# Performance work log

Hardware: AMD Instinct MI355X
Metric: run time of the kernel (lower is better)

## Reference

```python
import jax, jax.numpy as jnp
import numpy as np

D, H, W = 40, 32, 88
BEV_H, BEV_W = 125, 125
X_MIN, X_MAX, DX = -50.0, 50.0, 0.8
Y_MIN, Y_MAX, DY = -50.0, 50.0, 0.8
Z_MIN, DZ = -10.0, 20.0


def _voxel_indices():
    """Replicates frustum creation + get_geometry + index computation.
    Returns (flat_idx, valid) each of shape (D, H, W). Faithful to the
    original's sequential in-place max() semantics."""
    # depth_grid = arange(1, 41, 1) + 1  -> 2..41
    depth = jnp.arange(1.0, 41.0, 1.0) + 1.0            # (D,)
    xs = jnp.linspace(0.0, W - 1.0, W)                  # (W,)
    ys = jnp.linspace(0.0, H - 1.0, H)                  # (H,)
    d = depth[:, None, None]                            # (D,1,1)
    xd = jnp.broadcast_to(xs[None, None, :] * d, (D, H, W))  # x*depth
    yd = jnp.broadcast_to(ys[None, :, None] * d, (D, H, W))  # y*depth
    zd = jnp.broadcast_to(d, (D, H, W))                       # depth
    # first points_d.max(): over columns (xd, yd, zd)
    max1 = jnp.maximum(xd.max(), jnp.maximum(yd.max(), zd.max()))
    gx = xd / max1 * (X_MAX - X_MIN) + X_MIN
    # second points_d.max(): column 0 was overwritten in-place by gx
    max2 = jnp.maximum(gx.max(), jnp.maximum(yd.max(), zd.max()))
    gy = yd / max2 * (Y_MAX - Y_MIN) + Y_MIN
    gz = zd
    # voxelize (torch .long() truncates; all values here are >= 0)
    ix = ((gx - X_MIN) / DX).astype(jnp.int32)
    iy = ((gy - Y_MIN) / DY).astype(jnp.int32)
    iz = ((gz - Z_MIN) / DZ).astype(jnp.int32)
    valid = (ix >= 0) & (ix < BEV_W) & (iy >= 0) & (iy < BEV_H) & (iz >= 0)
    flat_idx = jnp.where(valid, iy * BEV_W + ix, 0)
    return flat_idx, valid


def setup_inputs() -> dict:
    key = jax.random.key(0)
    k1, k2, k3, k4, k5 = jax.random.split(key, 5)
    B, N, C = 1, 6, 128
    return {
        "img_feat": jax.random.normal(k1, (B, N, C, H, W), dtype=jnp.float32),
        "depth_logits": jax.random.normal(k2, (B, N, D, H, W), dtype=jnp.float32),
        "rots": jax.random.normal(k3, (B, N, 3, 3), dtype=jnp.float32),
        "trans": jax.random.normal(k4, (B, N, 3), dtype=jnp.float32),
        "intrins": jax.random.normal(k5, (B, N, 3, 3), dtype=jnp.float32),
    }


def reference(img_feat, depth_logits, rots, trans, intrins):
    B, N, C, h, w = img_feat.shape
    depth_probs = jax.nn.softmax(depth_logits, axis=2)         # (B,N,D,H,W)
    # depth-weighted outer product: (B,N,D,H,W,C)
    feats = jnp.einsum('bnchw,bndhw->bndhwc', img_feat, depth_probs)
    flat_feats = feats.reshape(-1, C)                          # (B*N*D*H*W, C)
    flat_idx, valid = _voxel_indices()                         # (D,H,W)
    idx = jnp.broadcast_to(flat_idx[None, None], (B, N, D, h, w)).reshape(-1)
    msk = jnp.broadcast_to(valid[None, None], (B, N, D, h, w)).reshape(-1)
    flat_feats = jnp.where(msk[:, None], flat_feats, 0.0)
    bev = jax.ops.segment_sum(flat_feats, idx, num_segments=BEV_H * BEV_W)
    bev = bev.reshape(BEV_H, BEV_W, C)
    return jnp.transpose(bev, (2, 0, 1))[None]                 # (1, C, 125, 125)
```

## Files before the change

### kernel.cpp

```cpp
#include <hip/hip_runtime.h>


constexpr int D = 40, H = 32, W = 88, HW = H * W;
constexpr int C = 128, NCAM = 6;
constexpr int BEV = 125, NBINS = BEV * BEV;
constexpr int NCOLS = NCAM * HW;

typedef __attribute__((ext_vector_type(8))) unsigned short us8;
typedef __attribute__((ext_vector_type(4))) float f4;
typedef __attribute__((ext_vector_type(2))) float f2;

__device__ __forceinline__ unsigned short f2bf(float x) {
    unsigned u = __float_as_uint(x);
    return (unsigned short)((u + 0x7FFF + ((u >> 16) & 1)) >> 16);
}
__device__ __forceinline__ float b2f(unsigned short u) {
    return __uint_as_float(((unsigned)u) << 16);
}

struct Tabs { short XP[D][126]; short YP[D][126]; };
constexpr Tabs make_tabs() {
    Tabs t{};
    for (int d = 0; d < D; ++d) {
        int dep = d + 2;
        int cntx[126] = {};
        for (int w = 0; w < W; ++w) {
            float gx = (float)(w * dep) / 3567.0f * 100.0f - 50.0f;
            int ix = (int)((gx + 50.0f) / 0.8f);
            if (ix < 125) cntx[ix]++;
        }
        t.XP[d][0] = 0;
        for (int X = 0; X < 125; ++X) t.XP[d][X + 1] = (short)(t.XP[d][X] + cntx[X]);
        int cnty[126] = {};
        for (int h = 0; h < H; ++h) {
            float gy = (float)(h * dep) / 1271.0f * 100.0f - 50.0f;
            int iy = (int)((gy + 50.0f) / 0.8f);
            if (iy < 125) cnty[iy]++;
        }
        t.YP[d][0] = 0;
        for (int Y = 0; Y < 125; ++Y) t.YP[d][Y + 1] = (short)(t.YP[d][Y] + cnty[Y]);
    }
    return t;
}
constexpr Tabs g_tabs = make_tabs();
__device__ const Tabs g_tab = g_tabs;

struct SegTable { unsigned a[4096]; unsigned b[4096]; int n; };

constexpr SegTable make_segs() {
    SegTable S{};
    int ns = 0;
    for (int iy = 0; iy < 125; ++iy) {
        int cnt[125] = {};
        for (int d = 0; d < D; ++d) {
            int yc = g_tabs.YP[d][iy + 1] - g_tabs.YP[d][iy];
            if (yc == 0) continue;
            for (int X = 0; X < 125; ++X)
                cnt[X] += (g_tabs.XP[d][X + 1] - g_tabs.XP[d][X]) * yc;
        }
        int X = 0;
        while (X < 125) {
            if (cnt[X] > 176) {
                int d0 = 0;
                while (d0 < D) {
                    int run = 0, d1 = d0;
                    while (d1 < D) {
                        int piece = (g_tabs.XP[d1][X + 1] - g_tabs.XP[d1][X]) *
                                    (g_tabs.YP[d1][iy + 1] - g_tabs.YP[d1][iy]);
                        if (d1 > d0 && run + piece > 128) break;
                        run += piece; ++d1;
                    }
                    if (run > 0) {
                        S.a[ns] = ((unsigned)iy << 16) | ((unsigned)X << 8) | (unsigned)(X + 1);
                        S.b[ns] = (1u << 31) | ((unsigned)d0 << 25) | ((unsigned)d1 << 19) | (unsigned)run;
                        ++ns;
                    }
                    d0 = d1;
                }
                ++X;
            } else {
                int X0 = X, run = 0;
                while (X < 125 && (X - X0) < 16 && cnt[X] <= 176 &&
                       (X == X0 || run + cnt[X] <= 128)) {
                    run += cnt[X]; ++X;
                }
                if (run > 0) {
                    S.a[ns] = ((unsigned)iy << 16) | ((unsigned)X0 << 8) | (unsigned)X;
                    S.b[ns] = ((unsigned)0 << 25) | ((unsigned)D << 19) | (unsigned)run;
                    ++ns;
                }
            }
        }
    }
    S.n = ns;
    return S;
}
constexpr SegTable g_raw = make_segs();

constexpr SegTable reorder_segs() {
    SegTable R{};
    int pos = 0;
    for (int i = 0; i < g_raw.n; ++i)
        if ((int)(g_raw.b[i] & 0x7FFFF) >= 120) { R.a[pos] = g_raw.a[i]; R.b[pos] = g_raw.b[i]; ++pos; }
    for (int i = 0; i < g_raw.n; ++i)
        if ((int)(g_raw.b[i] & 0x7FFFF) <  120) { R.a[pos] = g_raw.a[i]; R.b[pos] = g_raw.b[i]; ++pos; }
    R.n = pos;
    return R;
}
constexpr SegTable g_ct = reorder_segs();
constexpr int NSEG = g_ct.n;
static_assert(NSEG > 0 && NSEG <= 4096, "seg table overflow");
__device__ const SegTable g_segs = g_ct;

struct Meta { unsigned m[4096]; int ne; };
constexpr Meta make_meta() {
    Meta M{};
    int pos = 0;
    for (int i = 0; i < NSEG; ++i) {
        int cnt = (int)(g_ct.b[i] & 0x7FFFF);
        int ng = (((cnt + 1) >> 1) + 3) >> 2;
        M.m[i] = (g_ct.b[i] & 0x80000000u) | ((unsigned)pos << 10) | (unsigned)ng;
        pos += 2 * ng * 4;
    }
    M.ne = pos;
    return M;
}
constexpr Meta g_mt = make_meta();
constexpr int NE_TOT = g_mt.ne;
static_assert(NE_TOT < (1 << 21), "start field overflow");
struct MetaArr { unsigned m[4096]; };
constexpr MetaArr make_meta_arr() { MetaArr A{}; for (int i = 0; i < 4096; ++i) A.m[i] = g_mt.m[i]; return A; }
__device__ const MetaArr g_metaD = make_meta_arr();

__device__ __align__(16) unsigned g_glist[NE_TOT + 64];

constexpr int SMAX_BLOCKS  = NCOLS / 256;
constexpr int BUILD_BLOCKS = (NSEG + 3) / 4;
constexpr int PACK_BLOCKS  = (C / 8) * (HW / 32);
constexpr int ZERO_TOTAL   = C * NBINS / 4;
constexpr int ZERO_BLOCKS  = (ZERO_TOTAL + 1023) / 1024;
constexpr int MEGA_BLOCKS  = SMAX_BLOCKS + BUILD_BLOCKS + PACK_BLOCKS + ZERO_BLOCKS;

__global__ void __launch_bounds__(256) mega_kernel(
        const float* __restrict__ feat,
        const float* __restrict__ logits,
        float* __restrict__ probs_t,
        unsigned short* __restrict__ feat_p,
        float* __restrict__ out) {
    __shared__ __align__(16) float tile[NCAM * 8 * 37];
    int b = blockIdx.x, t = threadIdx.x;

    if (b < SMAX_BLOCKS) {
        int col = b * 256 + t;
        int n  = col / HW;
        int hw = col - n * HW;
        const float* src = logits + ((size_t)n * D) * HW + hw;
        float m = -3.402823466e+38f;
#pragma unroll 20
        for (int d = 0; d < D; ++d)
            m = fmaxf(m, src[(size_t)d * HW]);
        float s = 0.f;
#pragma unroll 8
        for (int d = 0; d < D; ++d)
            s += expf(src[(size_t)d * HW] - m);
        float inv = 1.0f / s;
#pragma unroll 8
        for (int d = 0; d < D; ++d)
            probs_t[(size_t)((d << 12) | hw) * 8 + n] =
                expf(src[(size_t)d * HW] - m) * inv;

    } else if (b < SMAX_BLOCKS + BUILD_BLOCKS) {
        int slot = (b - SMAX_BLOCKS) * 4 + (t >> 6);
        int lane = t & 63;
        if (slot < NSEG) {
            unsigned da = g_segs.a[slot], db = g_segs.b[slot], mb = g_metaD.m[slot];
            int iy = (int)(da >> 16), X0 = (int)((da >> 8) & 0xFF), X1 = (int)(da & 0xFF);
            int d0 = (int)((db >> 25) & 0x3F), d1 = (int)((db >> 19) & 0x3F);
            int drange = d1 - d0;
            int ng4 = (int)(mb & 0x3FFu) * 4;
            unsigned* gl = g_glist + ((mb >> 10) & 0x1FFFFFu);
            int base = 0;
            for (int bl = 0; bl < X1 - X0; ++bl) {
                int d = d0 + lane;
                int hb = 0, he = 0, wb = 0, we = 0, cnt = 0;
                if (lane < drange) {
                    hb = g_tab.YP[d][iy];      he = g_tab.YP[d][iy + 1];
                    wb = g_tab.XP[d][X0 + bl]; we = g_tab.XP[d][X0 + bl + 1];
                    cnt = (he - hb) * (we - wb);
                }
                int inc = cnt;
#pragma unroll
                for (int delta = 1; delta < 64; delta <<= 1) {
                    int y = __shfl_up(inc, delta, 64);
                    if (lane >= delta) inc += y;
                }
                int tot = __shfl(inc, 63, 64);
                int o = base + inc - cnt;
                int run_end = base + tot;
                for (int h = hb; h < he; ++h)
                    for (int w = wb; w < we; ++w) {
                        unsigned v = ((unsigned)bl << 19) | ((unsigned)d << 12)
                                   | (unsigned)(h * W + w);
                        if (o >= run_end - 2) v |= 0x80000000u;
                        gl[(o & 1) * ng4 + (o >> 1)] = v;
                        ++o;
                    }
                base = run_end;
            }
            int m = base;
#pragma unroll
            for (int dg = 0; dg < 2; ++dg) {
                int cnt2 = (m + 1 - dg) >> 1;
                for (int k = cnt2 + lane; k < ng4; k += 64)
                    gl[dg * ng4 + k] = (16u << 19) | 0x80000000u;
            }
        }

    } else if (b < SMAX_BLOCKS + BUILD_BLOCKS + PACK_BLOCKS) {
        int bb = b - SMAX_BLOCKS - BUILD_BLOCKS;
        int c0  = (bb / 88) * 8;
        int hw0 = (bb % 88) * 32;
        int cq = t >> 5, hwL = t & 31;
#pragma unroll
        for (int n = 0; n < NCAM; ++n)
            tile[(n * 8 + cq) * 37 + hwL] =
                feat[((size_t)(n * C + c0 + cq)) * HW + hw0 + hwL];
        __syncthreads();
        int hl = t >> 3, cL = t & 7;
        us8 v;
#pragma unroll
        for (int n = 0; n < NCAM; ++n)
            v[n] = f2bf(tile[(n * 8 + cL) * 37 + hl]);
        v[6] = 0; v[7] = 0;
        *(us8*)(feat_p + ((size_t)(hw0 + hl) * C + (c0 + cL)) * 8) = v;

    } else {
        int base = (b - SMAX_BLOCKS - BUILD_BLOCKS - PACK_BLOCKS) * 1024;
#pragma unroll
        for (int k = 0; k < 4; ++k) {
            int i = base + k * 256 + t;
            if (i < ZERO_TOTAL) ((f4*)out)[i] = f4{0.f, 0.f, 0.f, 0.f};
        }
    }
}

__global__ void __launch_bounds__(128, 4) gather_kernel(
        const unsigned short* __restrict__ feat_p,
        const float* __restrict__ probs_t,
        float* __restrict__ out) {
    __shared__ __align__(16) float T[2][17][66];
    __shared__ __align__(16) unsigned EL[192];
    int t = threadIdx.x;
    int slot = blockIdx.x >> 1, chalf = blockIdx.x & 1;
    unsigned da = g_segs.a[slot], mb = g_metaD.m[slot];
    int iy = (int)(da >> 16), X0 = (int)((da >> 8) & 0xFF), X1 = (int)(da & 0xFF);
    int width = X1 - X0;
    bool split = (mb >> 31) != 0;
    int ng = (int)(mb & 0x3FFu);
    unsigned start = (mb >> 10) & 0x1FFFFFu;
    int dg = __builtin_amdgcn_readfirstlane((int)(threadIdx.x >> 6));
    int lane = t & 63;
    int c = chalf * 64 + lane;
    int ntot = ng * 8;

    if (t < ntot) EL[t] = g_glist[start + (unsigned)t];
    if (t + 128 < ntot) EL[t + 128] = g_glist[start + (unsigned)(t + 128)];
    { float* Tf = &T[0][0][0];
      for (int i = t; i < 2 * 17 * 66; i += 128) Tf[i] = 0.f; }
    __syncthreads();

    const unsigned* ep = EL + dg * ng * 4;
    const unsigned short* fbase = feat_p + (size_t)c * 8;
    float* Tp = &T[dg][0][0];
    float racc = 0.f;

#define LOADE(E, g_) { uint4 ee_ = *(const uint4*)(ep + 4 * (g_));            \
    E[0] = (unsigned)__builtin_amdgcn_readfirstlane((int)ee_.x);              \
    E[1] = (unsigned)__builtin_amdgcn_readfirstlane((int)ee_.y);              \
    E[2] = (unsigned)__builtin_amdgcn_readfirstlane((int)ee_.z);              \
    E[3] = (unsigned)__builtin_amdgcn_readfirstlane((int)ee_.w); }
#define ISSUE(S, E) _Pragma("unroll") for (int i_ = 0; i_ < 4; ++i_) {        \
    fv##S[i_] = *(const us8*)(fbase + ((size_t)(E[i_] & 0xFFFu) << 10));      \
    const float* pp_ = probs_t + ((size_t)(E[i_] & 0x3FFFFu) << 3);           \
    pa##S[i_] = *(const f4*)pp_; pb##S[i_] = *(const f2*)(pp_ + 4); }
#define CONS(S, E) _Pragma("unroll") for (int i_ = 0; i_ < 4; ++i_) {         \
    racc += pa##S[i_].x * b2f(fv##S[i_][0]) + pa##S[i_].y * b2f(fv##S[i_][1]) \
          + pa##S[i_].z * b2f(fv##S[i_][2]) + pa##S[i_].w * b2f(fv##S[i_][3]) \
          + pb##S[i_].x * b2f(fv##S[i_][4]) + pb##S[i_].y * b2f(fv##S[i_][5]);\
    if (E[i_] & 0x80000000u) {                                                \
        Tp[((E[i_] >> 19) & 31u) * 66 + (unsigned)lane] += racc; racc = 0.f; } }

    unsigned EA[4], EB[4], ET[4];
    us8 fvA[4], fvB[4];
    f4 paA[4], paB[4];
    f2 pbA[4], pbB[4];
    LOADE(EA, 0); LOADE(EB, 1);
    ISSUE(A, EA);
    int g = 0;
    for (; g + 2 <= ng; g += 2) {
        ISSUE(B, EB);
        LOADE(ET, g + 2);
        CONS(A, EA);
        if (g + 2 < ng) {
            ISSUE(A, ET);
#pragma unroll
            for (int q = 0; q < 4; ++q) EA[q] = ET[q];
        }
        CONS(B, EB);
        LOADE(EB, g + 3);
    }
    if (g < ng) CONS(A, EA);
#undef LOADE
#undef ISSUE
#undef CONS
    __syncthreads();

    int binbase = iy * BEV + X0;
#pragma unroll
    for (int it = 0; it < 8; ++it) {
        int bl = t & 15, cc = it * 8 + (t >> 4);
        if (bl < width) {
            float v = T[0][bl][cc] + T[1][bl][cc];
            float* dst = &out[(size_t)(chalf * 64 + cc) * NBINS + binbase + bl];
            if (split) atomicAdd(dst, v);
            else       *dst = v;
        }
    }
}

extern "C" void kernel_launch(void* const* d_in, const int* in_sizes, int n_in,
                              void* d_out, int out_size, void* d_ws, size_t ws_size,
                              hipStream_t stream) {
    const float* img_feat     = (const float*)d_in[0];
    const float* depth_logits = (const float*)d_in[1];
    float* out = (float*)d_out;

    char* p = (char*)d_ws;
    float*          probs_t = (float*)p;          p += (size_t)D * 4096 * 8 * 4;
    unsigned short* feat_p  = (unsigned short*)p; p += (size_t)HW * C * 8 * 2;

    mega_kernel<<<MEGA_BLOCKS, 256, 0, stream>>>(
        img_feat, depth_logits, probs_t, feat_p, out);
    gather_kernel<<<NSEG * 2, 128, 0, stream>>>(feat_p, probs_t, out);
}
```

Measured before the change: 107.8 us.

## Pack bf16 features to 12 bytes and triple-buffer gather loads

```diff
diff --git a/kernel.cpp b/kernel.cpp
--- a/kernel.cpp
+++ b/kernel.cpp
@@ -13,9 +13,6 @@
 __device__ __forceinline__ unsigned short f2bf(float x) {
     unsigned u = __float_as_uint(x);
     return (unsigned short)((u + 0x7FFF + ((u >> 16) & 1)) >> 16);
-}
-__device__ __forceinline__ float b2f(unsigned short u) {
-    return __uint_as_float(((unsigned)u) << 16);
 }
 
 struct Tabs { short XP[D][126]; short YP[D][126]; };
@@ -227,12 +224,15 @@
                 feat[((size_t)(n * C + c0 + cq)) * HW + hw0 + hwL];
         __syncthreads();
         int hl = t >> 3, cL = t & 7;
-        us8 v;
+        unsigned short v[6];
 #pragma unroll
         for (int n = 0; n < NCAM; ++n)
             v[n] = f2bf(tile[(n * 8 + cL) * 37 + hl]);
-        v[6] = 0; v[7] = 0;
-        *(us8*)(feat_p + ((size_t)(hw0 + hl) * C + (c0 + cL)) * 8) = v;
+        unsigned* dst = (unsigned*)(feat_p +
+            ((size_t)(hw0 + hl) * C + (c0 + cL)) * 6);
+        dst[0] = (unsigned)v[0] | ((unsigned)v[1] << 16);
+        dst[1] = (unsigned)v[2] | ((unsigned)v[3] << 16);
+        dst[2] = (unsigned)v[4] | ((unsigned)v[5] << 16);
 
     } else {
         int base = (b - SMAX_BLOCKS - BUILD_BLOCKS - PACK_BLOCKS) * 1024;
@@ -244,7 +244,7 @@
     }
 }
 
-__global__ void __launch_bounds__(128, 4) gather_kernel(
+__global__ void __launch_bounds__(128, 2) gather_kernel(
         const unsigned short* __restrict__ feat_p,
         const float* __restrict__ probs_t,
         float* __restrict__ out) {
@@ -270,7 +270,7 @@
     __syncthreads();
 
     const unsigned* ep = EL + dg * ng * 4;
-    const unsigned short* fbase = feat_p + (size_t)c * 8;
+    const char* fbase = (const char*)feat_p + (size_t)c * 12;
     float* Tp = &T[dg][0][0];
     float racc = 0.f;
 
@@ -280,36 +280,43 @@
     E[2] = (unsigned)__builtin_amdgcn_readfirstlane((int)ee_.z);              \
     E[3] = (unsigned)__builtin_amdgcn_readfirstlane((int)ee_.w); }
 #define ISSUE(S, E) _Pragma("unroll") for (int i_ = 0; i_ < 4; ++i_) {        \
-    fv##S[i_] = *(const us8*)(fbase + ((size_t)(E[i_] & 0xFFFu) << 10));      \
+    const unsigned* fp_ = (const unsigned*)(fbase +                           \
+                          (size_t)(E[i_] & 0xFFFu) * 1536);                   \
+    fv##S[i_][0] = fp_[0]; fv##S[i_][1] = fp_[1]; fv##S[i_][2] = fp_[2];      \
     const float* pp_ = probs_t + ((size_t)(E[i_] & 0x3FFFFu) << 3);           \
     pa##S[i_] = *(const f4*)pp_; pb##S[i_] = *(const f2*)(pp_ + 4); }
 #define CONS(S, E) _Pragma("unroll") for (int i_ = 0; i_ < 4; ++i_) {         \
-    racc += pa##S[i_].x * b2f(fv##S[i_][0]) + pa##S[i_].y * b2f(fv##S[i_][1]) \
-          + pa##S[i_].z * b2f(fv##S[i_][2]) + pa##S[i_].w * b2f(fv##S[i_][3]) \
-          + pb##S[i_].x * b2f(fv##S[i_][4]) + pb##S[i_].y * b2f(fv##S[i_][5]);\
+    unsigned u0_ = fv##S[i_][0], u1_ = fv##S[i_][1], u2_ = fv##S[i_][2];      \
+    racc += pa##S[i_].x * __uint_as_float(u0_ << 16)                          \
+          + pa##S[i_].y * __uint_as_float(u0_ & 0xFFFF0000u)                  \
+          + pa##S[i_].z * __uint_as_float(u1_ << 16)                          \
+          + pa##S[i_].w * __uint_as_float(u1_ & 0xFFFF0000u)                  \
+          + pb##S[i_].x * __uint_as_float(u2_ << 16)                          \
+          + pb##S[i_].y * __uint_as_float(u2_ & 0xFFFF0000u);                 \
     if (E[i_] & 0x80000000u) {                                                \
         Tp[((E[i_] >> 19) & 31u) * 66 + (unsigned)lane] += racc; racc = 0.f; } }
 
-    unsigned EA[4], EB[4], ET[4];
-    us8 fvA[4], fvB[4];
-    f4 paA[4], paB[4];
-    f2 pbA[4], pbB[4];
-    LOADE(EA, 0); LOADE(EB, 1);
-    ISSUE(A, EA);
+    unsigned EA[4], EB[4], EC[4];
+    unsigned fvA[4][3], fvB[4][3], fvC[4][3];
+    f4 paA[4], paB[4], paC[4];
+    f2 pbA[4], pbB[4], pbC[4];
+    LOADE(EA, 0); ISSUE(A, EA);
+    LOADE(EB, 1); ISSUE(B, EB);
+    LOADE(EC, 2);
     int g = 0;
-    for (; g + 2 <= ng; g += 2) {
-        ISSUE(B, EB);
-        LOADE(ET, g + 2);
+    for (; g + 3 <= ng; g += 3) {
+        ISSUE(C, EC);
         CONS(A, EA);
-        if (g + 2 < ng) {
-            ISSUE(A, ET);
-#pragma unroll
-            for (int q = 0; q < 4; ++q) EA[q] = ET[q];
-        }
+        LOADE(EA, g + 3); ISSUE(A, EA);
         CONS(B, EB);
-        LOADE(EB, g + 3);
-    }
-    if (g < ng) CONS(A, EA);
+        LOADE(EB, g + 4); ISSUE(B, EB);
+        CONS(C, EC);
+        LOADE(EC, g + 5);
+    }
+    if (g + 2 < ng) ISSUE(C, EC);
+    if (g     < ng) CONS(A, EA);
+    if (g + 1 < ng) CONS(B, EB);
+    if (g + 2 < ng) CONS(C, EC);
 #undef LOADE
 #undef ISSUE
 #undef CONS
@@ -337,7 +344,7 @@
 
     char* p = (char*)d_ws;
     float*          probs_t = (float*)p;          p += (size_t)D * 4096 * 8 * 4;
-    unsigned short* feat_p  = (unsigned short*)p; p += (size_t)HW * C * 8 * 2;
+    unsigned short* feat_p  = (unsigned short*)p; p += (size_t)HW * C * 6 * 2;
 
     mega_kernel<<<MEGA_BLOCKS, 256, 0, stream>>>(
         img_feat, depth_logits, probs_t, feat_p, out);
```

New measurement: 106.3 us. No clear change (-1.5%).
